# Optimization experiments

Measured on AMD Instinct MI355X. Metric: run time of the kernel, lower is better.

Reference implementation:

```python
import jax, jax.numpy as jnp
import numpy as np

B, F_IN, GRID, D, C = 32768, 64, 8, 16, 10
N = GRID * GRID          # 64 nodes
HID = N * D              # 1024
ATOMS = 2
LN_EPS = 1e-5
EPS = 1e-8


def _layernorm(h):
    mu = h.mean(-1, keepdims=True)
    var = h.var(-1, keepdims=True)
    return (h - mu) / jnp.sqrt(var + LN_EPS)


def _regulator(sig, w1, b1, g, be, w2, b2):
    # Linear -> LayerNorm -> Tanh -> Linear -> Sigmoid
    h = jnp.tanh(_layernorm(sig @ w1.T + b1) * g + be)
    return jax.nn.sigmoid(h @ w2.T + b2)


def _reg_params(key, in_dim):
    k = jax.random.split(key, 4)
    return (jax.random.normal(k[0], (16, in_dim)) * 0.3,
            jax.random.normal(k[1], (16,)) * 0.1,
            jnp.ones((16,)), jnp.zeros((16,)),
            jax.random.normal(k[2], (3, 16)) * 0.3,
            jax.random.normal(k[3], (3,)) * 0.1)


def setup_inputs() -> dict:
    key = jax.random.key(0)
    ks = jax.random.split(key, 16)
    # 2D grid 4-neighbour adjacency mask (constant)
    mask = np.zeros((N, N), np.float32)
    for i in range(N):
        r, c = divmod(i, GRID)
        if r > 0: mask[i, i - GRID] = 1
        if r < GRID - 1: mask[i, i + GRID] = 1
        if c > 0: mask[i, i - 1] = 1
        if c < GRID - 1: mask[i, i + 1] = 1
    pr = _reg_params(ks[10], 3)
    cr = _reg_params(ks[11], 3)
    sr = _reg_params(ks[12], 3)
    scr = _reg_params(ks[13], 2)
    inp = {
        "x": jax.random.normal(ks[0], (B, F_IN)),
        "W_embed": jax.random.normal(ks[1], (HID, F_IN)) * 0.1,
        "b_embed": jnp.zeros((HID,)),
        "adj_weights": jax.random.normal(ks[2], (N, N)) * 0.1,
        "adj_mask": jnp.asarray(mask),
        "V_slow": jax.random.normal(ks[3], (D, D)) * 0.1,
        "W_slow": jax.random.normal(ks[4], (D, D)) * 0.1,
        "gate_w": jax.random.normal(ks[5], (1, D)) * 0.3,
        "gate_b": jnp.zeros((1,)),
        "W_fast": jax.random.normal(ks[6], (D, D)) * 0.05,  # buffer, eval mode (no Hebbian update)
        "basis": jax.random.normal(ks[7], (ATOMS, D)) * 0.5,
        "Wq": jax.random.normal(ks[8], (D, D)) * 0.2,
        "sc_w1": jax.random.normal(ks[9], (8, HID)) * 0.05,
        "sc_w2": jax.random.normal(ks[14], (4, 8)) * 0.3,
        "W_read": jax.random.normal(ks[15], (C, HID)) * 0.05,
        "b_read": jnp.zeros((C,)),
    }
    for pre, p in (("pr", pr), ("cr", cr), ("sr", sr), ("scr", scr)):
        for nm, v in zip(("w1", "b1", "g", "be", "w2", "b2"), p):
            inp[pre + "_" + nm] = v
    return inp


def reference(x, W_embed, b_embed, adj_weights, adj_mask,
              pr_w1, pr_b1, pr_g, pr_be, pr_w2, pr_b2,
              V_slow, W_slow, gate_w, gate_b, W_fast,
              cr_w1, cr_b1, cr_g, cr_be, cr_w2, cr_b2,
              basis, Wq,
              sr_w1, sr_b1, sr_g, sr_be, sr_w2, sr_b2,
              sc_w1, sc_w2,
              scr_w1, scr_b1, scr_g, scr_be, scr_w2, scr_b2,
              W_read, b_read):
    Bx = x.shape[0]
    x_embed = (x @ W_embed.T + b_embed).reshape(Bx, N, D)

    # --- AutoregulatedPlasticity adjacency ---
    sig = jnp.stack([jnp.var(x, ddof=1), jnp.abs(x_embed).mean(),
                     jnp.linalg.norm(adj_weights)])[None]
    pl = _regulator(sig, pr_w1, pr_b1, pr_g, pr_be, pr_w2, pr_b2)[0]
    adj = jax.nn.sigmoid(adj_weights * pl[0]) * adj_mask
    adj = adj / jnp.clip(adj.sum(1, keepdims=True), 1e-6, None)
    x_agg = jnp.einsum('nm,bmd->bnd', adj, x_embed)

    # --- AutoregulatedContinuum (eval: W_fast fixed) ---
    xf = x_agg.reshape(-1, D)           # [B*N, D]
    v = xf @ V_slow.T
    sig = jnp.stack([jnp.var(xf, ddof=1), jnp.abs(v).mean(),
                     jnp.linalg.norm(W_slow)])[None]
    ctrl = _regulator(sig, cr_w1, cr_b1, cr_g, cr_be, cr_w2, cr_b2)[0]
    gate = jax.nn.sigmoid(v @ gate_w.T + gate_b) * ctrl[0]   # [B*N, 1]
    fast_out = xf @ W_fast.T
    x_proc = (gate * (v + fast_out * ctrl[2])).reshape(Bx, N, D)

    # --- AutoregulatedSymbiotic, applied per node (vmapped over node axis) ---
    ortho = jnp.linalg.norm(basis @ basis.T - jnp.eye(ATOMS))
    scale = D ** 0.5 + EPS

    def sym_one(xn):  # xn: [B, D]
        w = jax.nn.softmax((xn @ Wq.T) @ basis.T / scale, axis=-1)  # [B, ATOMS]
        ent = -(w * jnp.log(w + EPS)).sum(-1).mean()
        sig_n = jnp.stack([jnp.var(xn, ddof=1), ent, ortho])[None]
        infl = _regulator(sig_n, sr_w1, sr_b1, sr_g, sr_be, sr_w2, sr_b2)[0, 0]
        return (1.0 - infl) * xn + infl * (w @ basis), ent

    refined, ents = jax.vmap(sym_one)(x_proc.transpose(1, 0, 2))  # [N,B,D]
    x_proc = refined.transpose(1, 0, 2)
    entropy = ents[-1]  # torch loop keeps the last node's entropy

    x_flat = x_proc.reshape(Bx, HID)
    logits = x_flat @ W_read.T + b_read

    # --- AutoregulatedSupConHead (entropy.item() -> detached scalar) ---
    sigc = jnp.stack([jnp.var(x_flat, ddof=1),
                      jax.lax.stop_gradient(entropy)])[None]
    gain = _regulator(sigc, scr_w1, scr_b1, scr_g, scr_be, scr_w2, scr_b2)[0, 0]
    proj = (jax.nn.relu(x_flat @ sc_w1.T) @ sc_w2.T) * gain
    return logits, proj, entropy, ortho
```

## Files before the change

kernel.cpp:

```cpp
#include <hip/hip_runtime.h>

typedef unsigned short u16;
typedef __attribute__((ext_vector_type(8))) short short8;
typedef __attribute__((ext_vector_type(4))) float f32x4;

#define MFMA16(a,b,c) __builtin_amdgcn_mfma_f32_16x16x32_bf16(a,b,c,0,0,0)

#define B_SZ   32768
#define NNODE  64
#define NB_PAIR (B_SZ*NNODE)
#define OUT_PROJ   327680
#define OUT_ENT    458752
#define OUT_ORTHO  458753

#define OFF_SCAL   ((size_t)0)
#define OFF_ADJ    ((size_t)512)
#define OFF_BEFF   (OFF_ADJ  + 8192u)
#define OFF_WEFF   (OFF_BEFF + 4096u)
#define OFF_WCAT   (OFF_WEFF + 131072u)
#define OFF_S1     (OFF_WCAT + 65536u)
#define OFF_S2     (OFF_S1   + 12288u)
#define OFF_S3     (OFF_S2   + 12288u)
#define OFF_S4     (OFF_S3   + 2048u*192u*4u)
#define OFF_H      (OFF_S4   + 8192u)
#define OFF_W01    (OFF_H    + (size_t)B_SZ*8u*4u)
#define OFF_CAN    (OFF_W01  + (size_t)NB_PAIR*2u*4u)

#define CAN_X      0u
#define CAN_WEMB   2097152u
#define CAN_WREAD  (CAN_WEMB + 65536u)
#define CAN_SCW1   (CAN_WREAD + 10240u)
#define CAN_SMALL  (CAN_SCW1 + 8192u)
#define CAN_TOTAL  (CAN_SMALL + 11008u)
#define OFF_BEX    (((OFF_CAN + (size_t)CAN_TOTAL*2u) + 63u) & ~(size_t)63u)
#define OFF_WET    (OFF_BEX + 48u*16u*2u)
#define OFF_VW     (OFF_WET + 131072u)
#define OFF_VB     (OFF_VW  + 131072u)
#define OFF_WC     (OFF_VB  + 4096u)
#define OFF_SW     (OFF_WC  + 131072u)
#define OFF_BC2    (OFF_SW  + 24576u)
#define OFF_SB     (OFF_BC2 + 4096u)
#define OFF_DR     (OFF_SB  + 1024u)
#define WS_NEEDED  (OFF_DR  + 192u*8u)

__device__ __forceinline__ float bf2f(u16 u){
    unsigned v = ((unsigned)u) << 16;
    return __builtin_bit_cast(float, v);
}
__device__ __forceinline__ u16 f2bf(float f){
    unsigned u = __builtin_bit_cast(unsigned, f);
    u += 0x7FFFu + ((u >> 16) & 1u);
    return (u16)(u >> 16);
}
__device__ __forceinline__ float sigm(float x){ return 1.f/(1.f + expf(-x)); }
__device__ __forceinline__ u16 conv_one(const void* src, int i, int isfp32){
    return isfp32 ? f2bf(((const float*)src)[i]) : ((const u16*)src)[i];
}
__device__ __forceinline__ void store_out(void* dout, int idx, float v, int isfp32){
    if (isfp32) ((float*)dout)[idx] = v;
    else        ((u16*)dout)[idx]   = f2bf(v);
}
__device__ __forceinline__ double blk_red(double v, double* sred, int tid){
    #pragma unroll
    for (int off = 32; off > 0; off >>= 1) v += __shfl_xor(v, off);
    if ((tid & 63) == 0) sred[tid >> 6] = v;
    __syncthreads();
    double r = sred[0] + sred[1] + sred[2] + sred[3];
    __syncthreads();
    return r;
}

__device__ void run_regulator(const u16* w1, const u16* b1, const u16* g,
                              const u16* be, const u16* w2, const u16* b2,
                              const float* sig, int in_dim, float* out)
{
    float h[16];
    float mu = 0.f;
    for (int i = 0; i < 16; ++i){
        float a = bf2f(b1[i]);
        for (int j = 0; j < in_dim; ++j) a += sig[j]*bf2f(w1[i*in_dim + j]);
        h[i] = a; mu += a;
    }
    mu *= 0.0625f;
    float var = 0.f;
    for (int i = 0; i < 16; ++i){ float d = h[i]-mu; var += d*d; }
    var *= 0.0625f;
    float inv = 1.f / sqrtf(var + 1e-5f);
    for (int i = 0; i < 16; ++i){
        float hn = (h[i]-mu)*inv;
        h[i] = tanhf(hn*bf2f(g[i]) + bf2f(be[i]));
    }
    for (int c = 0; c < 3; ++c){
        float o = bf2f(b2[c]);
        for (int i = 0; i < 16; ++i) o += h[i]*bf2f(w2[c*16 + i]);
        out[c] = sigm(o);
    }
}

__global__ __launch_bounds__(256) void kp_probe(const u16* xraw, float* scal)
{
    __shared__ int red[4];
    int tid = threadIdx.x, wave = tid>>6, lane = tid&63;
    int c = 0;
    #pragma unroll
    for (int j = 0; j < 4; ++j){
        u16 u = xraw[(tid*4 + j)*2];
        int e = (u >> 7) & 0xFF;
        if (u == 0 || (e >= 90 && e <= 140)) c++;
    }
    #pragma unroll
    for (int off = 32; off > 0; off >>= 1) c += __shfl_xor(c, off);
    if (lane == 0) red[wave] = c;
    __syncthreads();
    if (tid == 0){
        int tot = red[0]+red[1]+red[2]+red[3];
        scal[127] = (tot < 614) ? 1.0f : 0.0f;
    }
}

__global__ __launch_bounds__(256) void kc_big(const void* x, const void* wemb,
    const void* wread, const void* scw1, u16* can, const float* scal)
{
    int isfp32 = scal[127] != 0.f;
    int gid = blockIdx.x*256 + threadIdx.x, stride = gridDim.x*256;
    for (int i = gid; i < 2097152; i += stride) can[CAN_X + i]     = conv_one(x, i, isfp32);
    for (int i = gid; i < 65536;   i += stride) can[CAN_WEMB + i]  = conv_one(wemb, i, isfp32);
    for (int i = gid; i < 10240;   i += stride) can[CAN_WREAD + i] = conv_one(wread, i, isfp32);
    for (int i = gid; i < 8192;    i += stride) can[CAN_SCW1 + i]  = conv_one(scw1, i, isfp32);
}

struct SmallTab { const void* src[36]; int cnt[36]; int off[36]; };
__global__ __launch_bounds__(256) void kc_small(SmallTab t, u16* can, const float* scal)
{
    int isfp32 = scal[127] != 0.f;
    int gid = blockIdx.x*256 + threadIdx.x, stride = gridDim.x*256;
    for (int e = 0; e < 36; ++e){
        const void* s = t.src[e];
        u16* d = can + t.off[e];
        int n = t.cnt[e];
        for (int i = gid; i < n; i += stride) d[i] = conv_one(s, i, isfp32);
    }
}

__global__ __launch_bounds__(256) void k0_wcat(const u16* wread, const u16* scw1,
    const u16* wemb, const u16* vslow, const u16* gatew, u16* wcat, u16* wembT, u16* bex)
{
    int b = blockIdx.x, tid = threadIdx.x;
    if (b < 128){
        int idx = b*256 + tid;
        int row = idx >> 10, k = idx & 1023;
        u16 v = 0;
        if (row < 10)      v = wread[row*1024 + k];
        else if (row < 18) v = scw1[(row-10)*1024 + k];
        wcat[idx] = v;
    } else if (b < 384){
        int idx = (b-128)*256 + tid;
        int m = idx >> 10, jj = idx & 1023;
        wembT[jj*64 + m] = wemb[m*1024 + jj];
    } else {
        if (tid < 16){
            float a = 0.f;
            for (int i = 0; i < 16; ++i) a += bf2f(gatew[i])*bf2f(vslow[i*16+tid]);
            bex[32*16+tid] = f2bf(a);
        }
    }
}

__global__ __launch_bounds__(256) void k1_embed(const u16* x, const u16* wemb,
                                                const u16* bemb, float* s1)
{
    __shared__ float red[12];
    int tid = threadIdx.x, wave = tid>>6, lane = tid&63;
    int m = lane&15, quad = lane>>4;
    int cg = blockIdx.x & 31, rc = blockIdx.x >> 5;
    int col0 = cg*32 + m, col1 = col0 + 16;
    short8 b00 = *(const short8*)(wemb + col0*64 + quad*8);
    short8 b01 = *(const short8*)(wemb + col0*64 + quad*8 + 32);
    short8 b10 = *(const short8*)(wemb + col1*64 + quad*8);
    short8 b11 = *(const short8*)(wemb + col1*64 + quad*8 + 32);
    float bias0 = bf2f(bemb[col0]), bias1 = bf2f(bemb[col1]);
    float sx = 0.f, sxx = 0.f, sabs = 0.f;
    const u16* xbase = x + (size_t)(rc*1024 + wave*256 + m)*64 + quad*8;
    #pragma unroll 4
    for (int it = 0; it < 16; ++it){
        const u16* xr = xbase + (size_t)it*16*64;
        short8 a0 = *(const short8*)xr;
        short8 a1 = *(const short8*)(xr + 32);
        if (cg == 0){
            #pragma unroll
            for (int j = 0; j < 8; ++j){
                float f0 = bf2f((u16)a0[j]); sx += f0; sxx += f0*f0;
                float f1 = bf2f((u16)a1[j]); sx += f1; sxx += f1*f1;
            }
        }
        f32x4 zc = {0.f,0.f,0.f,0.f};
        f32x4 c0 = MFMA16(a0, b00, zc);
        c0 = MFMA16(a1, b01, c0);
        f32x4 c1 = MFMA16(a0, b10, zc);
        c1 = MFMA16(a1, b11, c1);
        #pragma unroll
        for (int r = 0; r < 4; ++r)
            sabs += fabsf(c0[r]+bias0) + fabsf(c1[r]+bias1);
    }
    #pragma unroll
    for (int off = 32; off > 0; off >>= 1){
        sx   += __shfl_xor(sx, off);
        sxx  += __shfl_xor(sxx, off);
        sabs += __shfl_xor(sabs, off);
    }
    if (lane == 0){ red[wave*3] = sx; red[wave*3+1] = sxx; red[wave*3+2] = sabs; }
    __syncthreads();
    if (tid == 0){
        for (int k = 0; k < 3; ++k)
            s1[blockIdx.x*3 + k] = red[k] + red[3+k] + red[6+k] + red[9+k];
    }
}

__global__ __launch_bounds__(256) void k2_adj(const u16* adjw, const u16* adjm, const u16* bemb,
    const u16* w1, const u16* b1, const u16* g, const u16* be, const u16* w2, const u16* b2,
    const float* s1, float* scal, u16* adjb, float* beff)
{
    __shared__ double sred[4];
    __shared__ float raw[4096];
    __shared__ float rowsum[64];
    __shared__ float bembs[1024];
    __shared__ float pl0s;
    int tid = threadIdx.x;
    for (int i = tid; i < 1024; i += 256) bembs[i] = bf2f(bemb[i]);
    double s=0, ss=0, sa=0;
    for (int i = tid; i < 1024; i += 256){
        s += (double)s1[i*3]; ss += (double)s1[i*3+1]; sa += (double)s1[i*3+2];
    }
    double nq = 0;
    for (int i = tid; i < 4096; i += 256){ float f = bf2f(adjw[i]); nq += (double)(f*f); }
    double S  = blk_red(s,  sred, tid);
    double SS = blk_red(ss, sred, tid);
    double SA = blk_red(sa, sred, tid);
    double NQ = blk_red(nq, sred, tid);
    if (tid == 0){
        double nx = 2097152.0;
        float sg[3];
        sg[0] = (float)((SS - S*S/nx)/(nx - 1.0));
        sg[1] = (float)(SA / 33554432.0);
        sg[2] = sqrtf((float)NQ);
        float o[3];
        run_regulator(w1,b1,g,be,w2,b2, sg, 3, o);
        scal[0] = o[0]; pl0s = o[0];
    }
    __syncthreads();
    float pl0 = pl0s;
    for (int i = tid; i < 4096; i += 256)
        raw[i] = sigm(bf2f(adjw[i])*pl0) * bf2f(adjm[i]);
    __syncthreads();
    if (tid < 64){
        float r = 0.f;
        for (int mc = 0; mc < 64; ++mc) r += raw[tid*64 + mc];
        rowsum[tid] = fmaxf(r, 1e-6f);
    }
    __syncthreads();
    for (int i = tid; i < 4096; i += 256) adjb[i] = f2bf(raw[i] / rowsum[i>>6]);
    for (int o = tid; o < 1024; o += 256){
        int n = o >> 4, d = o & 15;
        float a = 0.f;
        for (int m = 0; m < 64; ++m) a += raw[n*64+m]*bembs[m*16+d];
        beff[o] = a / rowsum[n];
    }
}

__global__ __launch_bounds__(256) void k2b_mfma(const u16* adjb, const u16* wembT, u16* weff)
{
    int tid = threadIdx.x, wave = tid>>6, lane = tid&63;
    int m = lane&15, quad = lane>>4;
    const u16* ar = adjb + (wave*16 + m)*64 + quad*8;
    short8 a0 = *(const short8*)ar;
    short8 a1 = *(const short8*)(ar + 32);
    int col = blockIdx.x*16 + m;
    const u16* br = wembT + col*64 + quad*8;
    short8 b0 = *(const short8*)br;
    short8 b1 = *(const short8*)(br + 32);
    f32x4 acc = {0.f,0.f,0.f,0.f};
    acc = MFMA16(a0, b0, acc);
    acc = MFMA16(a1, b1, acc);
    #pragma unroll
    for (int r = 0; r < 4; ++r)
        weff[(size_t)(wave*16 + quad*4 + r)*1024 + blockIdx.x*16 + m] = f2bf(acc[r]);
}

__global__ __launch_bounds__(256) void kvw(const u16* vslow, const u16* weff, const float* beff,
                                           u16* vw, float* vbias)
{
    __shared__ float Vs[256];
    int tid = threadIdx.x, b = blockIdx.x;
    Vs[tid] = bf2f(vslow[tid]);
    __syncthreads();
    if (b < 256){
        int idx = b*256 + tid;
        int j = idx >> 6, kf = idx & 63;
        int n = j >> 4, i = j & 15;
        float a = 0.f;
        #pragma unroll
        for (int d = 0; d < 16; ++d) a += Vs[i*16+d]*bf2f(weff[(size_t)(n*16+d)*64 + kf]);
        vw[(size_t)j*64 + kf] = f2bf(a);
    } else {
        int o = (b-256)*256 + tid;
        int n = o >> 4, i = o & 15;
        float a = 0.f;
        #pragma unroll
        for (int d = 0; d < 16; ++d) a += Vs[i*16+d]*beff[n*16+d];
        vbias[o] = a;
    }
}

__global__ __launch_bounds__(256) void k3_stats(const u16* x, const u16* weff, const float* beff,
                                                const u16* vw, const float* vbias, float* s2)
{
    __shared__ float red[12];
    int tid = threadIdx.x, wave = tid>>6, lane = tid&63;
    int m = lane&15, quad = lane>>4;
    int cg = blockIdx.x & 31, rc = blockIdx.x >> 5;
    int col0 = cg*32 + m, col1 = col0 + 16;
    short8 b00 = *(const short8*)(weff + (size_t)col0*64 + quad*8);
    short8 b01 = *(const short8*)(weff + (size_t)col0*64 + quad*8 + 32);
    short8 b10 = *(const short8*)(weff + (size_t)col1*64 + quad*8);
    short8 b11 = *(const short8*)(weff + (size_t)col1*64 + quad*8 + 32);
    short8 v00 = *(const short8*)(vw + (size_t)col0*64 + quad*8);
    short8 v01 = *(const short8*)(vw + (size_t)col0*64 + quad*8 + 32);
    short8 v10 = *(const short8*)(vw + (size_t)col1*64 + quad*8);
    short8 v11 = *(const short8*)(vw + (size_t)col1*64 + quad*8 + 32);
    float be0 = beff[col0], be1 = beff[col1];
    float vb0 = vbias[col0], vb1 = vbias[col1];
    float psum=0.f, pssq=0.f, pabsv=0.f;
    const u16* xbase = x + (size_t)(rc*1024 + wave*256 + m)*64 + quad*8;
    #pragma unroll 4
    for (int it = 0; it < 16; ++it){
        const u16* xr = xbase + (size_t)it*16*64;
        short8 a0 = *(const short8*)xr;
        short8 a1 = *(const short8*)(xr + 32);
        f32x4 zc = {0.f,0.f,0.f,0.f};
        f32x4 c0 = MFMA16(a0, b00, zc);
        c0 = MFMA16(a1, b01, c0);
        f32x4 c1 = MFMA16(a0, b10, zc);
        c1 = MFMA16(a1, b11, c1);
        f32x4 w0 = MFMA16(a0, v00, zc);
        w0 = MFMA16(a1, v01, w0);
        f32x4 w1 = MFMA16(a0, v10, zc);
        w1 = MFMA16(a1, v11, w1);
        #pragma unroll
        for (int r = 0; r < 4; ++r){
            float f0 = c0[r] + be0, f1 = c1[r] + be1;
            psum += f0 + f1; pssq += f0*f0 + f1*f1;
            pabsv += fabsf(w0[r] + vb0) + fabsf(w1[r] + vb1);
        }
    }
    #pragma unroll
    for (int off = 32; off > 0; off >>= 1){
        psum  += __shfl_xor(psum, off);
        pssq  += __shfl_xor(pssq, off);
        pabsv += __shfl_xor(pabsv, off);
    }
    if (lane == 0){ red[wave*3] = psum; red[wave*3+1] = pssq; red[wave*3+2] = pabsv; }
    __syncthreads();
    if (tid == 0){
        for (int k = 0; k < 3; ++k)
            s2[blockIdx.x*3 + k] = red[k] + red[3+k] + red[6+k] + red[9+k];
    }
}

__global__ __launch_bounds__(256) void k3b_ctrl(const u16* wslow,
    const u16* vslow, const u16* wfast, const u16* wq, const u16* basis,
    const u16* w1, const u16* b1, const u16* g, const u16* be, const u16* w2, const u16* b2,
    const float* s2, float* scal, u16* bex)
{
    __shared__ double sred[4];
    __shared__ float ctrl2s;
    int tid = threadIdx.x;
    double s=0, ss=0, sv=0;
    for (int i = tid; i < 1024; i += 256){
        s += (double)s2[i*3]; ss += (double)s2[i*3+1]; sv += (double)s2[i*3+2];
    }
    float wf = bf2f(wslow[tid]);
    double nq = (double)(wf*wf);
    double S  = blk_red(s,  sred, tid);
    double SS = blk_red(ss, sred, tid);
    double SV = blk_red(sv, sred, tid);
    double NQ = blk_red(nq, sred, tid);
    if (tid == 0){
        double M = 33554432.0;
        float sg[3];
        sg[0] = (float)((SS - S*S/M)/(M - 1.0));
        sg[1] = (float)(SV / M);
        sg[2] = sqrtf((float)NQ);
        float o[3];
        run_regulator(w1,b1,g,be,w2,b2, sg, 3, o);
        scal[1] = o[0]; scal[2] = o[2];
        ctrl2s = o[2];
    }
    __syncthreads();
    float ctrl2 = ctrl2s;
    if (tid < 64){
        #pragma unroll
        for (int j = 0; j < 4; ++j){
            int idx = tid*4 + j;
            int d = idx >> 4, k = idx & 15;
            bex[(16+d)*16+k] = f2bf(bf2f(vslow[idx]) + ctrl2*bf2f(wfast[idx]));
        }
    } else if (tid < 96){
        int a = (tid-64) >> 4, k = (tid-64) & 15;
        float e = 0.f;
        for (int d = 0; d < 16; ++d){
            float bq = 0.f;
            for (int j = 0; j < 16; ++j) bq += bf2f(basis[a*16+j])*bf2f(wq[j*16+d]);
            e += bq*(bf2f(vslow[d*16+k]) + ctrl2*bf2f(wfast[d*16+k]));
        }
        bex[(33+a)*16+k] = f2bf(0.25f*e);
    }
}

__global__ __launch_bounds__(256) void kbw(const u16* bex, const u16* weff, const float* beff,
                                           const u16* gateb, u16* wc, u16* sw,
                                           float* bc, float* sb)
{
    __shared__ float BcL[256], gvL[16], e0L[16], e1L[16];
    int tid = threadIdx.x;
    if (tid < 256) BcL[tid] = bf2f(bex[(16 + (tid>>4))*16 + (tid&15)]);
    if (tid < 16){
        gvL[tid] = bf2f(bex[32*16+tid]);
        e0L[tid] = bf2f(bex[33*16+tid]);
        e1L[tid] = bf2f(bex[34*16+tid]);
    }
    __syncthreads();
    int id = blockIdx.x*256 + tid;
    if (id < 65536){
        int col = id >> 6, k = id & 63;
        int n = col >> 4, d = col & 15;
        float a = 0.f;
        #pragma unroll
        for (int dd = 0; dd < 16; ++dd)
            a += BcL[d*16+dd]*bf2f(weff[(size_t)(n*16+dd)*64 + k]);
        wc[(size_t)col*64 + k] = f2bf(a);
    } else if (id < 77824){
        int j2 = id - 65536;
        int scol = j2 >> 6, k = j2 & 63;
        int n = scol/3, j = scol - n*3;
        const float* sr = (j==0) ? gvL : (j==1) ? e0L : e1L;
        float a = 0.f;
        #pragma unroll
        for (int dd = 0; dd < 16; ++dd)
            a += sr[dd]*bf2f(weff[(size_t)(n*16+dd)*64 + k]);
        sw[(size_t)scol*64 + k] = f2bf(a);
    } else if (id < 78848){
        int col = id - 77824;
        int n = col >> 4, d = col & 15;
        float a = 0.f;
        #pragma unroll
        for (int dd = 0; dd < 16; ++dd) a += BcL[d*16+dd]*beff[n*16+dd];
        bc[col] = a;
    } else if (id < 79040){
        int s = id - 78848;
        int n = s/3, j = s - n*3;
        const float* sr = (j==0) ? gvL : (j==1) ? e0L : e1L;
        float a = 0.f;
        #pragma unroll
        for (int dd = 0; dd < 16; ++dd) a += sr[dd]*beff[n*16+dd];
        if (j == 0) a += bf2f(gateb[0]);
        sb[s] = a;
    }
}

#define SCP 193
__global__ __launch_bounds__(256) void k4_stats(const u16* x, const u16* wc, const u16* sw,
    const float* bc, const float* sb, const float* scal, float* wbuf, float* s3)
{
    __shared__ float sc[16*SCP];
    __shared__ float gt[1024];
    __shared__ float entp[256];
    __shared__ float snode[128];
    int tid = threadIdx.x, wave = tid>>6, lane = tid&63;
    int m = lane&15, quad = lane>>4;
    int row0 = blockIdx.x*16;
    const u16* xr = x + (row0 + m)*64 + quad*8;
    short8 a0 = *(const short8*)xr;
    short8 a1 = *(const short8*)(xr + 32);
    float ctrl0 = scal[1];
    #pragma unroll
    for (int tt = 0; tt < 3; ++tt){
        int ct = wave*3 + tt;
        int scol = ct*16 + m;
        const u16* br = sw + (size_t)scol*64 + quad*8;
        short8 b0 = *(const short8*)br;
        short8 b1 = *(const short8*)(br + 32);
        f32x4 zc = {0.f,0.f,0.f,0.f};
        f32x4 c = MFMA16(a0, b0, zc);
        c = MFMA16(a1, b1, c);
        float sbv = sb[scol];
        #pragma unroll
        for (int r = 0; r < 4; ++r)
            sc[(quad*4+r)*SCP + scol] = c[r] + sbv;
    }
    __syncthreads();
    {
        int n = tid & 63, rgrp = tid >> 6;
        float ent = 0.f;
        #pragma unroll
        for (int rr = 0; rr < 4; ++rr){
            int row = rgrp*4 + rr;
            float gd  = sc[row*SCP + 3*n];
            float e0d = sc[row*SCP + 3*n + 1];
            float e1d = sc[row*SCP + 3*n + 2];
            float gate = ctrl0 / (1.f + __expf(-gd));
            float l0 = gate*e0d, l1 = gate*e1d;
            float w1v = 1.f/(1.f + __expf(l0 - l1));
            float w0v = 1.f - w1v;
            ent += -(w0v*__logf(w0v + 1e-8f) + w1v*__logf(w1v + 1e-8f));
            gt[row*64 + n] = gate;
            float2 wv; wv.x = gate; wv.y = w0v;
            *(float2*)(wbuf + (size_t)(row0 + row)*128 + n*2) = wv;
        }
        entp[tid] = ent;
    }
    __syncthreads();
    #pragma unroll
    for (int tt = 0; tt < 16; ++tt){
        int n = wave*16 + tt;
        int col = n*16 + m;
        const u16* br = wc + (size_t)col*64 + quad*8;
        short8 b0 = *(const short8*)br;
        short8 b1 = *(const short8*)(br + 32);
        f32x4 zc = {0.f,0.f,0.f,0.f};
        f32x4 c = MFMA16(a0, b0, zc);
        c = MFMA16(a1, b1, c);
        float bcv = bc[col];
        float ps = 0.f, pq = 0.f;
        #pragma unroll
        for (int r = 0; r < 4; ++r){
            float gate = gt[(quad*4+r)*64 + n];
            float xp = gate*(c[r] + bcv);
            ps += xp; pq += xp*xp;
        }
        #pragma unroll
        for (int off = 32; off > 0; off >>= 1){
            ps += __shfl_xor(ps, off);
            pq += __shfl_xor(pq, off);
        }
        if (lane == 0){ snode[n] = ps; snode[64+n] = pq; }
    }
    __syncthreads();
    if (tid < 192){
        float v;
        if (tid < 128) v = snode[tid];
        else { int n = tid-128; v = entp[n]+entp[64+n]+entp[128+n]+entp[192+n]; }
        s3[(size_t)blockIdx.x*192 + tid] = v;
    }
}

__global__ __launch_bounds__(256) void k5a_red(const float* s3, double* dred)
{
    __shared__ double sred[4];
    int tid = threadIdx.x, col = blockIdx.x;
    double a = 0;
    for (int i = tid; i < 2048; i += 256) a += (double)s3[(size_t)i*192 + col];
    #pragma unroll
    for (int off = 32; off > 0; off >>= 1) a += __shfl_xor(a, off);
    if ((tid & 63) == 0) sred[tid >> 6] = a;
    __syncthreads();
    if (tid == 0) dred[col] = sred[0]+sred[1]+sred[2]+sred[3];
}

__global__ __launch_bounds__(64) void k5b_infl(const u16* basis,
    const u16* w1, const u16* b1, const u16* g, const u16* be, const u16* w2, const u16* b2,
    const double* dred, float* scal, void* dout)
{
    int n = threadIdx.x;
    int isfp32 = scal[127] != 0.f;
    double sum = dred[n], ssq = dred[64+n], ent = dred[128+n];
    double Mn = 524288.0;
    float varn = (float)((ssq - sum*sum/Mn)/(Mn - 1.0));
    float entm = (float)(ent / 32768.0);
    float b0[16], b1v[16];
    for (int d = 0; d < 16; ++d){ b0[d] = bf2f(basis[d]); b1v[d] = bf2f(basis[16+d]); }
    float g00=0.f, g01=0.f, g11=0.f;
    for (int d = 0; d < 16; ++d){ g00 += b0[d]*b0[d]; g01 += b0[d]*b1v[d]; g11 += b1v[d]*b1v[d]; }
    float ortho = sqrtf((g00-1.f)*(g00-1.f) + 2.f*g01*g01 + (g11-1.f)*(g11-1.f));
    float sg[3] = {varn, entm, ortho};
    float o[3];
    run_regulator(w1,b1,g,be,w2,b2, sg, 3, o);
    scal[4+n] = o[0];
    if (n == 63){ scal[68] = entm;  store_out(dout, OUT_ENT,   entm,  isfp32); }
    if (n == 0) { scal[69] = ortho; store_out(dout, OUT_ORTHO, ortho, isfp32); }
}

#define XSP 132
__global__ __launch_bounds__(256) void k6_read(const u16* x, const float* wbuf,
    const u16* wc, const float* bc, const u16* wcat,
    const u16* basis, const u16* bread, const float* scal,
    void* dout, float* hbuf, float* s4)
{
    __shared__ unsigned gwP[64*65];
    __shared__ u16 xs[4*16*XSP];
    __shared__ float infl_s[64], b0s[16], b1s[16], brd[16];
    __shared__ float red[8];
    int tid = threadIdx.x;
    int isfp32 = scal[127] != 0.f;
    for (int i = tid; i < 4096; i += 256){
        float2 gw = *(const float2*)(wbuf + (size_t)blockIdx.x*8192 + i*2);
        gwP[(i >> 6)*65 + (i & 63)] = ((unsigned)f2bf(gw.y) << 16) | (unsigned)f2bf(gw.x);
    }
    if (tid < 64) infl_s[tid] = scal[4+tid];
    if (tid < 16){
        b0s[tid] = bf2f(basis[tid]);
        b1s[tid] = bf2f(basis[16+tid]);
        brd[tid] = (tid < 10) ? bf2f(bread[tid]) : 0.f;
    }
    __syncthreads();
    int wave = tid>>6, lane = tid&63;
    int m = lane&15, quad = lane>>4;
    int row = blockIdx.x*64 + wave*16 + m;
    const u16* xr = x + (size_t)row*64 + quad*8;
    short8 a0 = *(const short8*)xr;
    short8 a1 = *(const short8*)(xr + 32);
    u16* xsw = xs + wave*16*XSP;
    f32x4 acc0 = {0.f,0.f,0.f,0.f}, acc1 = {0.f,0.f,0.f,0.f};
    float psum = 0.f, pssq = 0.f;
    for (int c8 = 0; c8 < 8; ++c8){
        #pragma unroll
        for (int t = 0; t < 8; ++t){
            int n = c8*8 + t;
            int col = n*16 + m;
            const u16* br = wc + (size_t)col*64 + quad*8;
            short8 b0 = *(const short8*)br;
            short8 b1 = *(const short8*)(br + 32);
            f32x4 zc = {0.f,0.f,0.f,0.f};
            f32x4 c = MFMA16(a0, b0, zc);
            c = MFMA16(a1, b1, c);
            float bcv = bc[col];
            float fi = infl_s[n], om = 1.f - fi;
            #pragma unroll
            for (int r = 0; r < 4; ++r){
                unsigned gv = gwP[(wave*16 + quad*4 + r)*65 + n];
                float gate = bf2f((u16)(gv & 0xFFFFu));
                float w0v  = bf2f((u16)(gv >> 16));
                float xp = gate*(c[r] + bcv);
                float xf = om*xp + fi*(w0v*b0s[m] + (1.f-w0v)*b1s[m]);
                psum += xf; pssq += xf*xf;
                xsw[(quad*4+r)*XSP + t*16 + m] = f2bf(xf);
            }
        }
        #pragma unroll
        for (int kk = 0; kk < 4; ++kk){
            short8 af = *(const short8*)(xsw + m*XSP + kk*32 + quad*8);
            short8 bb0 = *(const short8*)(wcat + m*1024      + c8*128 + kk*32 + quad*8);
            short8 bb1 = *(const short8*)(wcat + (16+m)*1024 + c8*128 + kk*32 + quad*8);
            acc0 = MFMA16(af, bb0, acc0);
            acc1 = MFMA16(af, bb1, acc1);
        }
    }
    int rowbase = blockIdx.x*64 + wave*16 + quad*4;
    #pragma unroll
    for (int r = 0; r < 4; ++r){
        int rowg = rowbase + r;
        if (m < 10) store_out(dout, rowg*10 + m, acc0[r] + brd[m], isfp32);
        else        hbuf[rowg*8 + (m-10)] = fmaxf(acc0[r], 0.f);
        if (m < 2)  hbuf[rowg*8 + 6 + m]  = fmaxf(acc1[r], 0.f);
    }
    #pragma unroll
    for (int off = 32; off > 0; off >>= 1){
        psum += __shfl_xor(psum, off);
        pssq += __shfl_xor(pssq, off);
    }
    if (lane == 0){ red[wave] = psum; red[4+wave] = pssq; }
    __syncthreads();
    if (tid == 0){
        s4[blockIdx.x*2]   = red[0]+red[1]+red[2]+red[3];
        s4[blockIdx.x*2+1] = red[4]+red[5]+red[6]+red[7];
    }
}

__global__ __launch_bounds__(256) void k7_gain(
    const u16* w1, const u16* b1, const u16* g, const u16* be, const u16* w2, const u16* b2,
    const float* s4, float* scal)
{
    __shared__ double sred[4];
    int tid = threadIdx.x;
    double s=0, ss=0;
    for (int i = tid; i < 512; i += 256){ s += (double)s4[i*2]; ss += (double)s4[i*2+1]; }
    double S  = blk_red(s,  sred, tid);
    double SS = blk_red(ss, sred, tid);
    if (tid == 0){
        double M = 33554432.0;
        float sg[2];
        sg[0] = (float)((SS - S*S/M)/(M - 1.0));
        sg[1] = scal[68];
        float o[3];
        run_regulator(w1,b1,g,be,w2,b2, sg, 2, o);
        scal[3] = o[0];
    }
}

__global__ __launch_bounds__(256) void k8_proj(const float* hbuf, const u16* scw2,
                                               const float* scal, void* dout)
{
    __shared__ float w2s[32];
    int tid = threadIdx.x;
    int isfp32 = scal[127] != 0.f;
    if (tid < 32) w2s[tid] = bf2f(scw2[tid]);
    __syncthreads();
    int b = blockIdx.x*256 + tid;
    float gain = scal[3];
    const float* h = hbuf + (size_t)b*8;
    float hv[8];
    #pragma unroll
    for (int k = 0; k < 8; ++k) hv[k] = h[k];
    #pragma unroll
    for (int i = 0; i < 4; ++i){
        float o = 0.f;
        #pragma unroll
        for (int k = 0; k < 8; ++k) o += hv[k]*w2s[i*8+k];
        store_out(dout, OUT_PROJ + b*4 + i, o*gain, isfp32);
    }
}

extern "C" void kernel_launch(void* const* d_in, const int* in_sizes, int n_in,
                              void* d_out, int out_size, void* d_ws, size_t ws_size,
                              hipStream_t stream)
{
    if (ws_size < WS_NEEDED) return;

    char* ws = (char*)d_ws;
    float* scal  = (float*)(ws + OFF_SCAL);
    u16*   adjb  = (u16*)  (ws + OFF_ADJ);
    float* beff  = (float*)(ws + OFF_BEFF);
    u16*   weff  = (u16*)  (ws + OFF_WEFF);
    u16*   wcat  = (u16*)  (ws + OFF_WCAT);
    float* s1    = (float*)(ws + OFF_S1);
    float* s2    = (float*)(ws + OFF_S2);
    float* s3    = (float*)(ws + OFF_S3);
    float* s4    = (float*)(ws + OFF_S4);
    float* hbuf  = (float*)(ws + OFF_H);
    float* wbuf  = (float*)(ws + OFF_W01);
    u16*   can   = (u16*)  (ws + OFF_CAN);
    u16*   bex   = (u16*)  (ws + OFF_BEX);
    u16*   wembT = (u16*)  (ws + OFF_WET);
    u16*   vw    = (u16*)  (ws + OFF_VW);
    float* vbias = (float*)(ws + OFF_VB);
    u16*   wc    = (u16*)  (ws + OFF_WC);
    u16*   sw    = (u16*)  (ws + OFF_SW);
    float* bc    = (float*)(ws + OFF_BC2);
    float* sb    = (float*)(ws + OFF_SB);
    double* dred = (double*)(ws + OFF_DR);

    static const int sidx[36] = {2,3,4,5,6,7,8,9,10,11,13,15,
        16,17,18,19,20,21, 22,23,24,25,26,27, 28,29,30,31,32,33, 34,35,36,37,38,39};
    static const int scnt[36] = {1024,4096,4096,256,256,16,1,256,32,256,32,10,
        48,16,16,16,48,3, 48,16,16,16,48,3, 48,16,16,16,48,3, 32,16,16,16,48,3};
    SmallTab t;
    const u16* canp[40];
    {
        int off = (int)CAN_SMALL;
        for (int j = 0; j < 36; ++j){
            t.src[j] = d_in[sidx[j]];
            t.cnt[j] = scnt[j];
            t.off[j] = off;
            canp[sidx[j]] = can + off;
            off += (scnt[j] + 7) & ~7;
        }
    }
    canp[0]  = can + CAN_X;
    canp[1]  = can + CAN_WEMB;
    canp[12] = can + CAN_SCW1;
    canp[14] = can + CAN_WREAD;

    const u16* pr_[6]; const u16* cr_[6]; const u16* sr_[6]; const u16* sc_[6];
    for (int i = 0; i < 6; ++i){
        pr_[i] = canp[16+i]; cr_[i] = canp[22+i];
        sr_[i] = canp[28+i]; sc_[i] = canp[34+i];
    }

    kp_probe<<<1,   256, 0, stream>>>((const u16*)d_in[0], scal);
    kc_big  <<<1024,256, 0, stream>>>(d_in[0], d_in[1], d_in[14], d_in[12], can, scal);
    kc_small<<<16,  256, 0, stream>>>(t, can, scal);
    k0_wcat <<<385, 256, 0, stream>>>(canp[14], canp[12], canp[1], canp[5], canp[7],
                 wcat, wembT, bex);
    k1_embed<<<1024,256, 0, stream>>>(canp[0], canp[1], canp[2], s1);
    k2_adj  <<<1,   256, 0, stream>>>(canp[3], canp[4], canp[2],
                 pr_[0],pr_[1],pr_[2],pr_[3],pr_[4],pr_[5], s1, scal, adjb, beff);
    k2b_mfma<<<64,  256, 0, stream>>>(adjb, wembT, weff);
    kvw     <<<260, 256, 0, stream>>>(canp[5], weff, beff, vw, vbias);
    k3_stats<<<1024,256, 0, stream>>>(canp[0], weff, beff, vw, vbias, s2);
    k3b_ctrl<<<1,   256, 0, stream>>>(canp[6], canp[5], canp[9], canp[11], canp[10],
                 cr_[0],cr_[1],cr_[2],cr_[3],cr_[4],cr_[5], s2, scal, bex);
    kbw     <<<312, 256, 0, stream>>>(bex, weff, beff, canp[8], wc, sw, bc, sb);
    k4_stats<<<2048,256, 0, stream>>>(canp[0], wc, sw, bc, sb, scal, wbuf, s3);
    k5a_red <<<192, 256, 0, stream>>>(s3, dred);
    k5b_infl<<<1,   64,  0, stream>>>(canp[10],
                 sr_[0],sr_[1],sr_[2],sr_[3],sr_[4],sr_[5], dred, scal, d_out);
    k6_read <<<512, 256, 0, stream>>>(canp[0], wbuf, wc, bc, wcat, canp[10], canp[15],
                 scal, d_out, hbuf, s4);
    k7_gain <<<1,   256, 0, stream>>>(
                 sc_[0],sc_[1],sc_[2],sc_[3],sc_[4],sc_[5], s4, scal);
    k8_proj <<<128, 256, 0, stream>>>(hbuf, canp[13], scal, d_out);
}
```

Baseline: 355.2 us.

## Fuse probe and gain kernels, pack gate weights to bf16, split k6 across waves

Folds the dtype probe into every kc_big block and the gain regulator into every k8_proj block, removing two single-block launches. k4 now writes gate/w0 as packed bf16 pairs instead of float2, halving that intermediate buffer's traffic. k6_read now handles 32 rows per block with 1024 blocks, splitting node chunks between wave pairs and combining partial accumulators through shared memory. Costs are redundant probe and regulator work in each block and an extra barrier plus LDS reduction in k6.

```diff
diff --git a/kernel.cpp b/kernel.cpp
--- a/kernel.cpp
+++ b/kernel.cpp
@@ -24,7 +24,7 @@
 #define OFF_S4     (OFF_S3   + 2048u*192u*4u)
 #define OFF_H      (OFF_S4   + 8192u)
 #define OFF_W01    (OFF_H    + (size_t)B_SZ*8u*4u)
-#define OFF_CAN    (OFF_W01  + (size_t)NB_PAIR*2u*4u)
+#define OFF_CAN    (OFF_W01  + (size_t)NB_PAIR*4u)
 
 #define CAN_X      0u
 #define CAN_WEMB   2097152u
@@ -97,10 +97,8 @@
     }
 }
 
-__global__ __launch_bounds__(256) void kp_probe(const u16* xraw, float* scal)
-{
-    __shared__ int red[4];
-    int tid = threadIdx.x, wave = tid>>6, lane = tid&63;
+__device__ __forceinline__ int probe_isfp32(const u16* xraw, int tid, int* sred)
+{
     int c = 0;
     #pragma unroll
     for (int j = 0; j < 4; ++j){
@@ -110,19 +108,21 @@
     }
     #pragma unroll
     for (int off = 32; off > 0; off >>= 1) c += __shfl_xor(c, off);
-    if (lane == 0) red[wave] = c;
-    __syncthreads();
-    if (tid == 0){
-        int tot = red[0]+red[1]+red[2]+red[3];
-        scal[127] = (tot < 614) ? 1.0f : 0.0f;
-    }
+    if ((tid & 63) == 0) sred[tid >> 6] = c;
+    __syncthreads();
+    int tot = sred[0]+sred[1]+sred[2]+sred[3];
+    __syncthreads();
+    return tot < 614;
 }
 
 __global__ __launch_bounds__(256) void kc_big(const void* x, const void* wemb,
-    const void* wread, const void* scw1, u16* can, const float* scal)
-{
-    int isfp32 = scal[127] != 0.f;
-    int gid = blockIdx.x*256 + threadIdx.x, stride = gridDim.x*256;
+    const void* wread, const void* scw1, u16* can, float* scal)
+{
+    __shared__ int sred[4];
+    int tid = threadIdx.x;
+    int isfp32 = probe_isfp32((const u16*)x, tid, sred);
+    if (blockIdx.x == 0 && tid == 0) scal[127] = isfp32 ? 1.0f : 0.0f;
+    int gid = blockIdx.x*256 + tid, stride = gridDim.x*256;
     for (int i = gid; i < 2097152; i += stride) can[CAN_X + i]     = conv_one(x, i, isfp32);
     for (int i = gid; i < 65536;   i += stride) can[CAN_WEMB + i]  = conv_one(wemb, i, isfp32);
     for (int i = gid; i < 10240;   i += stride) can[CAN_WREAD + i] = conv_one(wread, i, isfp32);
@@ -469,7 +469,7 @@
 
 #define SCP 193
 __global__ __launch_bounds__(256) void k4_stats(const u16* x, const u16* wc, const u16* sw,
-    const float* bc, const float* sb, const float* scal, float* wbuf, float* s3)
+    const float* bc, const float* sb, const float* scal, unsigned* wpack, float* s3)
 {
     __shared__ float sc[16*SCP];
     __shared__ float gt[1024];
@@ -513,8 +513,8 @@
             float w0v = 1.f - w1v;
             ent += -(w0v*__logf(w0v + 1e-8f) + w1v*__logf(w1v + 1e-8f));
             gt[row*64 + n] = gate;
-            float2 wv; wv.x = gate; wv.y = w0v;
-            *(float2*)(wbuf + (size_t)(row0 + row)*128 + n*2) = wv;
+            wpack[(size_t)(row0 + row)*64 + n] =
+                ((unsigned)f2bf(w0v) << 16) | (unsigned)f2bf(gate);
         }
         entp[tid] = ent;
     }
@@ -590,21 +590,20 @@
 }
 
 #define XSP 132
-__global__ __launch_bounds__(256) void k6_read(const u16* x, const float* wbuf,
+__global__ __launch_bounds__(256) void k6_read(const u16* x, const unsigned* wpack,
     const u16* wc, const float* bc, const u16* wcat,
     const u16* basis, const u16* bread, const float* scal,
     void* dout, float* hbuf, float* s4)
 {
-    __shared__ unsigned gwP[64*65];
+    __shared__ unsigned gwP[32*65];
     __shared__ u16 xs[4*16*XSP];
+    __shared__ float comb[2*64*9];
     __shared__ float infl_s[64], b0s[16], b1s[16], brd[16];
     __shared__ float red[8];
     int tid = threadIdx.x;
     int isfp32 = scal[127] != 0.f;
-    for (int i = tid; i < 4096; i += 256){
-        float2 gw = *(const float2*)(wbuf + (size_t)blockIdx.x*8192 + i*2);
-        gwP[(i >> 6)*65 + (i & 63)] = ((unsigned)f2bf(gw.y) << 16) | (unsigned)f2bf(gw.x);
-    }
+    for (int i = tid; i < 2048; i += 256)
+        gwP[(i >> 6)*65 + (i & 63)] = wpack[(size_t)blockIdx.x*2048 + i];
     if (tid < 64) infl_s[tid] = scal[4+tid];
     if (tid < 16){
         b0s[tid] = bf2f(basis[tid]);
@@ -614,14 +613,16 @@
     __syncthreads();
     int wave = tid>>6, lane = tid&63;
     int m = lane&15, quad = lane>>4;
-    int row = blockIdx.x*64 + wave*16 + m;
+    int rowgrp = wave & 1, half = wave >> 1;
+    int row = blockIdx.x*32 + rowgrp*16 + m;
     const u16* xr = x + (size_t)row*64 + quad*8;
     short8 a0 = *(const short8*)xr;
     short8 a1 = *(const short8*)(xr + 32);
     u16* xsw = xs + wave*16*XSP;
     f32x4 acc0 = {0.f,0.f,0.f,0.f}, acc1 = {0.f,0.f,0.f,0.f};
     float psum = 0.f, pssq = 0.f;
-    for (int c8 = 0; c8 < 8; ++c8){
+    for (int cc = 0; cc < 4; ++cc){
+        int c8 = half*4 + cc;
         #pragma unroll
         for (int t = 0; t < 8; ++t){
             int n = c8*8 + t;
@@ -636,7 +637,7 @@
             float fi = infl_s[n], om = 1.f - fi;
             #pragma unroll
             for (int r = 0; r < 4; ++r){
-                unsigned gv = gwP[(wave*16 + quad*4 + r)*65 + n];
+                unsigned gv = gwP[(rowgrp*16 + quad*4 + r)*65 + n];
                 float gate = bf2f((u16)(gv & 0xFFFFu));
                 float w0v  = bf2f((u16)(gv >> 16));
                 float xp = gate*(c[r] + bcv);
@@ -654,13 +655,24 @@
             acc1 = MFMA16(af, bb1, acc1);
         }
     }
-    int rowbase = blockIdx.x*64 + wave*16 + quad*4;
-    #pragma unroll
-    for (int r = 0; r < 4; ++r){
-        int rowg = rowbase + r;
-        if (m < 10) store_out(dout, rowg*10 + m, acc0[r] + brd[m], isfp32);
-        else        hbuf[rowg*8 + (m-10)] = fmaxf(acc0[r], 0.f);
-        if (m < 2)  hbuf[rowg*8 + 6 + m]  = fmaxf(acc1[r], 0.f);
+    if (half){
+        float* cb = comb + (rowgrp*64 + lane)*9;
+        #pragma unroll
+        for (int r = 0; r < 4; ++r){ cb[r] = acc0[r]; cb[4+r] = acc1[r]; }
+    }
+    __syncthreads();
+    if (!half){
+        const float* cb = comb + (rowgrp*64 + lane)*9;
+        int rowbase = blockIdx.x*32 + rowgrp*16 + quad*4;
+        #pragma unroll
+        for (int r = 0; r < 4; ++r){
+            float o0 = acc0[r] + cb[r];
+            float o1 = acc1[r] + cb[4+r];
+            int rowg = rowbase + r;
+            if (m < 10) store_out(dout, rowg*10 + m, o0 + brd[m], isfp32);
+            else        hbuf[rowg*8 + (m-10)] = fmaxf(o0, 0.f);
+            if (m < 2)  hbuf[rowg*8 + 6 + m]  = fmaxf(o1, 0.f);
+        }
     }
     #pragma unroll
     for (int off = 32; off > 0; off >>= 1){
@@ -675,14 +687,18 @@
     }
 }
 
-__global__ __launch_bounds__(256) void k7_gain(
+__global__ __launch_bounds__(256) void k8_proj(const float* hbuf, const u16* scw2,
     const u16* w1, const u16* b1, const u16* g, const u16* be, const u16* w2, const u16* b2,
-    const float* s4, float* scal)
+    const float* s4, const float* scal, void* dout)
 {
     __shared__ double sred[4];
+    __shared__ float w2s[32];
+    __shared__ float gains;
     int tid = threadIdx.x;
+    int isfp32 = scal[127] != 0.f;
+    if (tid < 32) w2s[tid] = bf2f(scw2[tid]);
     double s=0, ss=0;
-    for (int i = tid; i < 512; i += 256){ s += (double)s4[i*2]; ss += (double)s4[i*2+1]; }
+    for (int i = tid; i < 1024; i += 256){ s += (double)s4[i*2]; ss += (double)s4[i*2+1]; }
     double S  = blk_red(s,  sred, tid);
     double SS = blk_red(ss, sred, tid);
     if (tid == 0){
@@ -692,20 +708,11 @@
         sg[1] = scal[68];
         float o[3];
         run_regulator(w1,b1,g,be,w2,b2, sg, 2, o);
-        scal[3] = o[0];
-    }
-}
-
-__global__ __launch_bounds__(256) void k8_proj(const float* hbuf, const u16* scw2,
-                                               const float* scal, void* dout)
-{
-    __shared__ float w2s[32];
-    int tid = threadIdx.x;
-    int isfp32 = scal[127] != 0.f;
-    if (tid < 32) w2s[tid] = bf2f(scw2[tid]);
-    __syncthreads();
+        gains = o[0];
+    }
+    __syncthreads();
+    float gain = gains;
     int b = blockIdx.x*256 + tid;
-    float gain = scal[3];
     const float* h = hbuf + (size_t)b*8;
     float hv[8];
     #pragma unroll
@@ -736,7 +743,7 @@
     float* s3    = (float*)(ws + OFF_S3);
     float* s4    = (float*)(ws + OFF_S4);
     float* hbuf  = (float*)(ws + OFF_H);
-    float* wbuf  = (float*)(ws + OFF_W01);
+    unsigned* wpack = (unsigned*)(ws + OFF_W01);
     u16*   can   = (u16*)  (ws + OFF_CAN);
     u16*   bex   = (u16*)  (ws + OFF_BEX);
     u16*   wembT = (u16*)  (ws + OFF_WET);
@@ -775,7 +782,6 @@
         sr_[i] = canp[28+i]; sc_[i] = canp[34+i];
     }
 
-    kp_probe<<<1,   256, 0, stream>>>((const u16*)d_in[0], scal);
     kc_big  <<<1024,256, 0, stream>>>(d_in[0], d_in[1], d_in[14], d_in[12], can, scal);
     kc_small<<<16,  256, 0, stream>>>(t, can, scal);
     k0_wcat <<<385, 256, 0, stream>>>(canp[14], canp[12], canp[1], canp[5], canp[7],
@@ -789,13 +795,12 @@
     k3b_ctrl<<<1,   256, 0, stream>>>(canp[6], canp[5], canp[9], canp[11], canp[10],
                  cr_[0],cr_[1],cr_[2],cr_[3],cr_[4],cr_[5], s2, scal, bex);
     kbw     <<<312, 256, 0, stream>>>(bex, weff, beff, canp[8], wc, sw, bc, sb);
-    k4_stats<<<2048,256, 0, stream>>>(canp[0], wc, sw, bc, sb, scal, wbuf, s3);
+    k4_stats<<<2048,256, 0, stream>>>(canp[0], wc, sw, bc, sb, scal, wpack, s3);
     k5a_red <<<192, 256, 0, stream>>>(s3, dred);
     k5b_infl<<<1,   64,  0, stream>>>(canp[10],
                  sr_[0],sr_[1],sr_[2],sr_[3],sr_[4],sr_[5], dred, scal, d_out);
-    k6_read <<<512, 256, 0, stream>>>(canp[0], wbuf, wc, bc, wcat, canp[10], canp[15],
+    k6_read <<<1024,256, 0, stream>>>(canp[0], wpack, wc, bc, wcat, canp[10], canp[15],
                  scal, d_out, hbuf, s4);
-    k7_gain <<<1,   256, 0, stream>>>(
-                 sc_[0],sc_[1],sc_[2],sc_[3],sc_[4],sc_[5], s4, scal);
-    k8_proj <<<128, 256, 0, stream>>>(hbuf, canp[13], scal, d_out);
-}
+    k8_proj <<<128, 256, 0, stream>>>(hbuf, canp[13],
+                 sc_[0],sc_[1],sc_[2],sc_[3],sc_[4],sc_[5], s4, scal, d_out);
+}
```

Measured after the change: 352.2 us. No clear change (-0.9%).
